# Kernel optimization log

Measured on AMD Instinct MI355X. Metric: run time of the kernel, lower is better.

## Reference

```python
import jax, jax.numpy as jnp
import numpy as np

B, N, C_IN = 32, 1024, 128
F0, F1, F2 = 64, 64, 64
OUT = 10
RATIOS = (0.8, 0.8)
EPS = 1e-5


def setup_inputs() -> dict:
    key = jax.random.key(0)
    ks = jax.random.split(key, 16)
    N_nodes = jax.random.randint(ks[0], (B,), N // 2, N + 1)
    mask = (jnp.arange(N)[None, :] < N_nodes[:, None]).astype(jnp.float32)
    x = jax.random.normal(ks[1], (B, N, C_IN), dtype=jnp.float32)
    # sparse-ish symmetric binary adjacency restricted to valid nodes
    A = (jax.random.uniform(ks[2], (B, N, N)) < 0.02).astype(jnp.float32)
    A = jnp.maximum(A, jnp.swapaxes(A, 1, 2))
    A = A * mask[:, :, None] * mask[:, None, :]
    def lin(k, fi, fo):
        b = 1.0 / np.sqrt(fi)
        kw, kb = jax.random.split(k)
        return (jax.random.uniform(kw, (fi, fo), minval=-b, maxval=b),
                jax.random.uniform(kb, (fo,), minval=-b, maxval=b))
    W0, b0 = lin(ks[3], C_IN, F0)
    W1, b1 = lin(ks[4], F0, F1)
    W2, b2 = lin(ks[5], F1, F2)
    bp0 = 1.0 / np.sqrt(F0)
    p0 = jax.random.uniform(ks[6], (F0, 1), minval=-bp0, maxval=bp0)
    bp1 = 1.0 / np.sqrt(F1)
    p1 = jax.random.uniform(ks[7], (F1, 1), minval=-bp1, maxval=bp1)
    Wfc, bfc = lin(ks[8], F2, OUT)
    return {"x": x, "A": A, "mask": mask, "N_nodes": N_nodes,
            "W0": W0, "b0": b0, "W1": W1, "b1": b1, "W2": W2, "b2": b2,
            "p0": p0, "p1": p1, "Wfc": Wfc, "bfc": bfc}


def _gconv(x, A, W, b):
    # Kipf-Welling normalized Laplacian conv, batched dense
    n = A.shape[1]
    A_hat = A + jnp.eye(n, dtype=A.dtype)[None]
    D = (jnp.sum(A_hat, axis=1) + EPS) ** -0.5  # [B,N]
    L = D[:, :, None] * A_hat * D[:, None, :]
    h = jnp.einsum('bnm,bmc->bnc', L, x) @ W + b
    return jax.nn.relu(h)


def _pool(x, A, mask, N_nodes, p, ratio):
    Bc, Nc, C = x.shape
    y = (x.reshape(Bc * Nc, C) @ p).reshape(Bc, Nc)
    y = y / jnp.sqrt(jnp.sum(p ** 2))
    N_remove = (N_nodes.astype(jnp.float32) * (1.0 - ratio)).astype(N_nodes.dtype)
    # remove the N_remove lowest-scoring valid nodes per graph
    y_eff = jnp.where(mask > 0, y, jnp.inf)
    ranks = jnp.argsort(jnp.argsort(y_eff, axis=1), axis=1)  # ascending rank
    new_mask = mask * (ranks >= N_remove[:, None]).astype(mask.dtype)
    x = x * jnp.tanh(y)[:, :, None] * new_mask[:, :, None]
    A = new_mask[:, :, None] * A * new_mask[:, None, :]
    return x, A, new_mask, N_nodes - N_remove


def reference(x, A, mask, N_nodes, W0, b0, W1, b1, W2, b2, p0, p1, Wfc, bfc):
    x = _gconv(x, A, W0, b0)
    x, A, mask, N_nodes = _pool(x, A, mask, N_nodes, p0, RATIOS[0])
    x = _gconv(x, A, W1, b1)
    x, A, mask, N_nodes = _pool(x, A, mask, N_nodes, p1, RATIOS[1])
    x = _gconv(x, A, W2, b2)
    x = jnp.max(x, axis=1)  # global max pool over nodes [B,F2]
    return x @ Wfc + bfc
```

## Files before the change

### kernel.cpp

```cpp
#include <hip/hip_runtime.h>
#include <cstdint>
#include <cstddef>

#define BB 32
#define NN 1024
#define CIN 128
#define FF 64
#define NOUT 10
#define CAP 128
#define EPSV 1e-5f

__global__ __launch_bounds__(256) void k_front(const float* __restrict__ A,
                                               const float* __restrict__ x,
                                               const float* __restrict__ W0,
                                               unsigned short* __restrict__ adj,
                                               int* __restrict__ cnt,
                                               float* __restrict__ c1,
                                               float* __restrict__ c2,
                                               float* __restrict__ T) {
    __shared__ __align__(16) float Wl[64 * 64];
    int tid = threadIdx.x;
    int wave = tid >> 6, lane = tid & 63;
    if (blockIdx.x >= 8192) {
        int gid = blockIdx.x - 8192;
        int b = gid & 31;
        int cch = gid >> 5;
        int row0 = (b << 10) + cch * 16;
        int rsub = lane >> 4, f0 = (lane & 15) * 4;
        int r = row0 + wave * 4 + rsub;
        const float4* xr = (const float4*)(x + (size_t)r * CIN);
        float4 acc = {0.f, 0.f, 0.f, 0.f};
#pragma unroll
        for (int kc = 0; kc < 2; ++kc) {
            if (kc) __syncthreads();
            for (int t = tid; t < 64 * 16; t += 256)
                ((float4*)Wl)[t] = ((const float4*)W0)[kc * 1024 + t];
            __syncthreads();
#pragma unroll 4
            for (int k4 = 0; k4 < 16; ++k4) {
                float4 xv = xr[kc * 16 + k4];
                float4 w0 = *(const float4*)&Wl[(k4 * 4 + 0) * 64 + f0];
                float4 w1 = *(const float4*)&Wl[(k4 * 4 + 1) * 64 + f0];
                float4 w2 = *(const float4*)&Wl[(k4 * 4 + 2) * 64 + f0];
                float4 w3 = *(const float4*)&Wl[(k4 * 4 + 3) * 64 + f0];
                acc.x += xv.x * w0.x; acc.y += xv.x * w0.y; acc.z += xv.x * w0.z; acc.w += xv.x * w0.w;
                acc.x += xv.y * w1.x; acc.y += xv.y * w1.y; acc.z += xv.y * w1.z; acc.w += xv.y * w1.w;
                acc.x += xv.z * w2.x; acc.y += xv.z * w2.y; acc.z += xv.z * w2.z; acc.w += xv.z * w2.w;
                acc.x += xv.w * w3.x; acc.y += xv.w * w3.y; acc.z += xv.w * w3.z; acc.w += xv.w * w3.w;
            }
        }
        *(float4*)&T[(size_t)r * 64 + f0] = acc;
    } else {
        unsigned short* adjs = ((unsigned short*)Wl) + wave * CAP;
        int r = blockIdx.x * 4 + wave;
        const float4* Arow = (const float4*)(A + (size_t)r * NN);
        float4 v0 = Arow[lane];
        float4 v1 = Arow[64 + lane];
        float4 v2 = Arow[128 + lane];
        float4 v3 = Arow[192 + lane];
        int c = 0;
        unsigned long long lt = (lane == 0) ? 0ULL : ((1ULL << lane) - 1ULL);
        float4 vv[4] = {v0, v1, v2, v3};
#pragma unroll
        for (int it = 0; it < 4; ++it) {
            float4 v = vv[it];
            int j0 = it * 256 + lane * 4;
            unsigned long long m0 = __ballot(v.x != 0.f);
            unsigned long long m1 = __ballot(v.y != 0.f);
            unsigned long long m2 = __ballot(v.z != 0.f);
            unsigned long long m3 = __ballot(v.w != 0.f);
            int before = __popcll(m0 & lt) + __popcll(m1 & lt) +
                         __popcll(m2 & lt) + __popcll(m3 & lt);
            int p = c + before;
            if (v.x != 0.f) { if (p < CAP) adjs[p] = (unsigned short)(j0 + 0); ++p; }
            if (v.y != 0.f) { if (p < CAP) adjs[p] = (unsigned short)(j0 + 1); ++p; }
            if (v.z != 0.f) { if (p < CAP) adjs[p] = (unsigned short)(j0 + 2); ++p; }
            if (v.w != 0.f) { if (p < CAP) adjs[p] = (unsigned short)(j0 + 3); ++p; }
            c += __popcll(m0) + __popcll(m1) + __popcll(m2) + __popcll(m3);
        }
        int cc = (c > CAP) ? CAP : c;
        uint32_t* dst = (uint32_t*)(adj + (size_t)r * CAP);
        if (lane * 2 < cc) dst[lane] = ((const uint32_t*)adjs)[lane];
        if (lane == 0) {
            cnt[r] = cc;
            float D = 1.0f / sqrtf((float)c + 1.0f + EPSV);
            c1[r] = D;
            c2[r] = D * D;
        }
    }
}

__global__ __launch_bounds__(256) void k_mid(const unsigned short* __restrict__ adj,
                                             const int* __restrict__ cnt,
                                             const float* __restrict__ nm,
                                             float* __restrict__ c1, float* __restrict__ c2,
                                             const float* __restrict__ Xin,
                                             const float* __restrict__ W,
                                             const float* __restrict__ y,
                                             float* __restrict__ T) {
    __shared__ __align__(16) float Wl[64 * 64];
    int tid = threadIdx.x;
    if (blockIdx.x >= 8192) {
        int gid = blockIdx.x - 8192;
        int b = gid & 31;
        int cch = gid >> 5;
        int row0 = (b << 10) + cch * 16;
        for (int t = tid; t < 64 * 16; t += 256)
            ((float4*)Wl)[t] = ((const float4*)W)[t];
        __syncthreads();
        int wave = tid >> 6, lane = tid & 63;
        int rsub = lane >> 4, f0 = (lane & 15) * 4;
        int r = row0 + wave * 4 + rsub;
        float sc = tanhf(y[r]) * nm[r];
        const float4* xr = (const float4*)(Xin + (size_t)r * 64);
        float4 acc = {0.f, 0.f, 0.f, 0.f};
#pragma unroll 4
        for (int k4 = 0; k4 < 16; ++k4) {
            float4 xv = xr[k4];
            float4 w0 = *(const float4*)&Wl[(k4 * 4 + 0) * 64 + f0];
            float4 w1 = *(const float4*)&Wl[(k4 * 4 + 1) * 64 + f0];
            float4 w2 = *(const float4*)&Wl[(k4 * 4 + 2) * 64 + f0];
            float4 w3 = *(const float4*)&Wl[(k4 * 4 + 3) * 64 + f0];
            acc.x += xv.x * w0.x; acc.y += xv.x * w0.y; acc.z += xv.x * w0.z; acc.w += xv.x * w0.w;
            acc.x += xv.y * w1.x; acc.y += xv.y * w1.y; acc.z += xv.y * w1.z; acc.w += xv.y * w1.w;
            acc.x += xv.z * w2.x; acc.y += xv.z * w2.y; acc.z += xv.z * w2.z; acc.w += xv.z * w2.w;
            acc.x += xv.w * w3.x; acc.y += xv.w * w3.y; acc.z += xv.w * w3.z; acc.w += xv.w * w3.w;
        }
        acc.x *= sc; acc.y *= sc; acc.z *= sc; acc.w *= sc;
        *(float4*)&T[(size_t)r * 64 + f0] = acc;
    } else {
        int wave = tid >> 6, lane = tid & 63;
        int r = blockIdx.x * 4 + wave;
        int b = r >> 10;
        const unsigned short* arow = adj + (size_t)r * CAP;
        const float* nmb = nm + (b << 10);
        int n = cnt[r];
        float s = 0.f;
        if (lane < n)      s  = nmb[arow[lane]];
        if (lane + 64 < n) s += nmb[arow[lane + 64]];
        for (int sh = 32; sh; sh >>= 1) s += __shfl_xor(s, sh, 64);
        if (lane == 0) {
            float m = nm[r];
            float D = 1.0f / sqrtf(m * s + 1.0f + EPSV);
            c1[r] = m * D;
            c2[r] = D * D;
        }
    }
}

__global__ __launch_bounds__(256) void k_spmm(const unsigned short* __restrict__ adj,
                                              const int* __restrict__ cnt,
                                              const float* __restrict__ c1,
                                              const float* __restrict__ c2,
                                              const float* __restrict__ T,
                                              const float* __restrict__ bias,
                                              float* __restrict__ X,
                                              const float* __restrict__ p,
                                              float* __restrict__ y,
                                              float* __restrict__ gmax) {
    __shared__ __align__(16) float c1s[NN];
    __shared__ float red[4][64];
    int b   = blockIdx.x & 31;
    int cch = blockIdx.x >> 5;
    int tid = threadIdx.x;
    ((float4*)c1s)[tid] = ((const float4*)(c1 + (b << 10)))[tid];
    __syncthreads();
    int wave = tid >> 6, lane = tid & 63;
    int r0 = (b << 10) + cch * 16 + wave * 4;
    const float* Tb = T + ((size_t)(b << 10) << 6);
    float bv = bias[lane];
    float pv = 0.f, ppinv = 0.f;
    if (p != nullptr) {
        pv = p[lane];
        float pp = pv * pv;
        for (int s = 32; s; s >>= 1) pp += __shfl_xor(pp, s, 64);
        ppinv = 1.0f / sqrtf(pp);
    }
    float vmax = 0.f;
#pragma unroll
    for (int rr = 0; rr < 4; ++rr) {
        int r = r0 + rr;
        const unsigned short* arow = adj + (size_t)r * CAP;
        int n = cnt[r];
        float acc0 = 0.f, acc1 = 0.f, acc2 = 0.f, acc3 = 0.f;
        int t = 0;
        for (; t + 4 <= n; t += 4) {
            ushort4 j4 = *(const ushort4*)(arow + t);
            acc0 += c1s[j4.x] * Tb[((int)j4.x << 6) + lane];
            acc1 += c1s[j4.y] * Tb[((int)j4.y << 6) + lane];
            acc2 += c1s[j4.z] * Tb[((int)j4.z << 6) + lane];
            acc3 += c1s[j4.w] * Tb[((int)j4.w << 6) + lane];
        }
        for (; t < n; ++t) {
            int j = arow[t];
            acc0 += c1s[j] * Tb[(j << 6) + lane];
        }
        float acc = (acc0 + acc1) + (acc2 + acc3);
        int rl = r & 1023;
        float o = c1s[rl] * acc + c2[r] * T[((size_t)r << 6) + lane] + bv;
        o = fmaxf(o, 0.f);
        if (X != nullptr) X[((size_t)r << 6) + lane] = o;
        if (p != nullptr) {
            float a = o * pv;
            for (int s = 32; s; s >>= 1) a += __shfl_xor(a, s, 64);
            if (lane == 0) y[r] = a * ppinv;
        }
        vmax = fmaxf(vmax, o);
    }
    if (gmax != nullptr) {
        red[wave][lane] = vmax;
        __syncthreads();
        if (wave == 0) {
            float m = fmaxf(fmaxf(red[0][lane], red[1][lane]),
                            fmaxf(red[2][lane], red[3][lane]));
            atomicMax((int*)&gmax[(b << 6) + lane], __float_as_int(m));
        }
    }
}

__global__ __launch_bounds__(256) void k_rank(const float* __restrict__ y,
                                              const float* __restrict__ maskSrc,
                                              const int* __restrict__ nsrc,
                                              float* __restrict__ nmOut,
                                              int* __restrict__ ncur) {
    __shared__ __align__(16) float yv[NN];
    int b = blockIdx.x >> 4;
    int sub = blockIdx.x & 15;
    int tid = threadIdx.x;
    const float INF = __builtin_inff();
    {
        float4 v = ((const float4*)(y + (b << 10)))[tid];
        float4 m = ((const float4*)(maskSrc + (b << 10)))[tid];
        v.x = (m.x > 0.f) ? v.x : INF;
        v.y = (m.y > 0.f) ? v.y : INF;
        v.z = (m.z > 0.f) ? v.z : INF;
        v.w = (m.w > 0.f) ? v.w : INF;
        ((float4*)yv)[tid] = v;
    }
    int n = nsrc[b];
    const float RM = (float)(1.0 - 0.8);
    int nrem = (int)((float)n * RM);
    if (sub == 0 && tid == 0) ncur[b] = n - nrem;
    __syncthreads();
    int i = (sub << 6) + (tid >> 2);
    int q = tid & 3;
    float yi = yv[i];
    int rank = 0;
    if (yi < INF) {
        const float4* jbase = (const float4*)yv + (q << 6);
        int j0 = q << 8;
#pragma unroll 8
        for (int t = 0; t < 64; ++t) {
            float4 a = jbase[t];
            int j = j0 + t * 4;
            rank += (a.x < yi || (a.x == yi && j     < i)) ? 1 : 0;
            rank += (a.y < yi || (a.y == yi && j + 1 < i)) ? 1 : 0;
            rank += (a.z < yi || (a.z == yi && j + 2 < i)) ? 1 : 0;
            rank += (a.w < yi || (a.w == yi && j + 3 < i)) ? 1 : 0;
        }
    }
    rank += __shfl_xor(rank, 1, 64);
    rank += __shfl_xor(rank, 2, 64);
    if (q == 0) {
        float nmv = (yi < INF && rank >= nrem) ? 1.f : 0.f;
        nmOut[(b << 10) + i] = nmv;
    }
}

__global__ __launch_bounds__(64) void k_fc(const float* __restrict__ gmax,
                                           const float* __restrict__ Wfc,
                                           const float* __restrict__ bfc,
                                           float* __restrict__ out) {
    __shared__ float gl[64];
    int b = blockIdx.x, lane = threadIdx.x;
    gl[lane] = gmax[(b << 6) + lane];
    __syncthreads();
    if (lane < NOUT) {
        float acc = bfc[lane];
        for (int k = 0; k < 64; ++k) acc += gl[k] * Wfc[k * NOUT + lane];
        out[b * NOUT + lane] = acc;
    }
}

extern "C" void kernel_launch(void* const* d_in, const int* in_sizes, int n_in,
                              void* d_out, int out_size, void* d_ws, size_t ws_size,
                              hipStream_t stream) {
    const float* x    = (const float*)d_in[0];
    const float* A    = (const float*)d_in[1];
    const float* mask = (const float*)d_in[2];
    const int*   Nn   = (const int*)d_in[3];
    const float* W0   = (const float*)d_in[4];
    const float* b0   = (const float*)d_in[5];
    const float* W1   = (const float*)d_in[6];
    const float* b1   = (const float*)d_in[7];
    const float* W2   = (const float*)d_in[8];
    const float* b2   = (const float*)d_in[9];
    const float* p0   = (const float*)d_in[10];
    const float* p1   = (const float*)d_in[11];
    const float* Wfc  = (const float*)d_in[12];
    const float* bfc  = (const float*)d_in[13];
    float* out = (float*)d_out;

    char* ws = (char*)d_ws;
    size_t off = 0;
    auto alloc = [&](size_t bytes) -> void* {
        void* p = ws + off;
        off = (off + bytes + 255) & ~(size_t)255;
        return p;
    };
    unsigned short* adj = (unsigned short*)alloc((size_t)BB * NN * CAP * 2);
    int*   cnt  = (int*)  alloc((size_t)BB * NN * 4);
    float* X    = (float*)alloc((size_t)BB * NN * 64 * 4);
    float* T    = (float*)alloc((size_t)BB * NN * 64 * 4);
    float* c1   = (float*)alloc((size_t)BB * NN * 4);
    float* c2   = (float*)alloc((size_t)BB * NN * 4);
    float* y    = (float*)alloc((size_t)BB * NN * 4);
    float* nm0  = (float*)alloc((size_t)BB * NN * 4);
    float* nm1  = (float*)alloc((size_t)BB * NN * 4);
    int*   nc0  = (int*)  alloc((size_t)BB * 4);
    int*   nc1  = (int*)  alloc((size_t)BB * 4);
    float* gmax = (float*)alloc((size_t)BB * 64 * 4);

    hipMemsetAsync(gmax, 0, (size_t)BB * 64 * 4, stream);
    k_front<<<8192 + 2048, 256, 0, stream>>>(A, x, W0, adj, cnt, c1, c2, T);
    k_spmm<<<2048, 256, 0, stream>>>(adj, cnt, c1, c2, T, b0, X, p0, y, nullptr);
    k_rank<<<BB * 16, 256, 0, stream>>>(y, mask, Nn, nm0, nc0);
    k_mid<<<8192 + 2048, 256, 0, stream>>>(adj, cnt, nm0, c1, c2, X, W1, y, T);
    k_spmm<<<2048, 256, 0, stream>>>(adj, cnt, c1, c2, T, b1, X, p1, y, nullptr);
    k_rank<<<BB * 16, 256, 0, stream>>>(y, nm0, nc0, nm1, nc1);
    k_mid<<<8192 + 2048, 256, 0, stream>>>(adj, cnt, nm1, c1, c2, X, W2, y, T);
    k_spmm<<<2048, 256, 0, stream>>>(adj, cnt, c1, c2, T, b2, nullptr, nullptr, nullptr, gmax);
    k_fc<<<BB, 64, 0, stream>>>(gmax, Wfc, bfc, out);
}
```

Measured before the change: 373.1 us.

## Read only upper triangle of symmetric adjacency and scatter mirrored edges atomically

The adjacency extraction now relies on A being symmetric. Each wave handles a pair of rows (i and 1023-i) so the work stays balanced, reads only columns j >= i, and writes the mirrored edge into row j's list through atomic counters. This roughly halves the dominant dense A read. The first-layer degree normalisation is now computed inside the first spmm from the counts, which removes the c1/c2 writes. The cost is many global atomics, and neighbour order within each row is no longer deterministic, so float summation order can change.

```diff
diff --git a/kernel.cpp b/kernel.cpp
--- a/kernel.cpp
+++ b/kernel.cpp
@@ -15,14 +15,12 @@
                                                const float* __restrict__ W0,
                                                unsigned short* __restrict__ adj,
                                                int* __restrict__ cnt,
-                                               float* __restrict__ c1,
-                                               float* __restrict__ c2,
                                                float* __restrict__ T) {
     __shared__ __align__(16) float Wl[64 * 64];
     int tid = threadIdx.x;
     int wave = tid >> 6, lane = tid & 63;
-    if (blockIdx.x >= 8192) {
-        int gid = blockIdx.x - 8192;
+    if (blockIdx.x >= 4096) {
+        int gid = blockIdx.x - 4096;
         int b = gid & 31;
         int cch = gid >> 5;
         int row0 = (b << 10) + cch * 16;
@@ -52,40 +50,52 @@
         *(float4*)&T[(size_t)r * 64 + f0] = acc;
     } else {
         unsigned short* adjs = ((unsigned short*)Wl) + wave * CAP;
-        int r = blockIdx.x * 4 + wave;
-        const float4* Arow = (const float4*)(A + (size_t)r * NN);
-        float4 v0 = Arow[lane];
-        float4 v1 = Arow[64 + lane];
-        float4 v2 = Arow[128 + lane];
-        float4 v3 = Arow[192 + lane];
-        int c = 0;
+        int pairIdx = blockIdx.x * 4 + wave;
+        int b = pairIdx >> 9;
+        int i0 = pairIdx & 511;
+        int rbase = b << 10;
         unsigned long long lt = (lane == 0) ? 0ULL : ((1ULL << lane) - 1ULL);
-        float4 vv[4] = {v0, v1, v2, v3};
 #pragma unroll
-        for (int it = 0; it < 4; ++it) {
-            float4 v = vv[it];
-            int j0 = it * 256 + lane * 4;
-            unsigned long long m0 = __ballot(v.x != 0.f);
-            unsigned long long m1 = __ballot(v.y != 0.f);
-            unsigned long long m2 = __ballot(v.z != 0.f);
-            unsigned long long m3 = __ballot(v.w != 0.f);
-            int before = __popcll(m0 & lt) + __popcll(m1 & lt) +
-                         __popcll(m2 & lt) + __popcll(m3 & lt);
-            int p = c + before;
-            if (v.x != 0.f) { if (p < CAP) adjs[p] = (unsigned short)(j0 + 0); ++p; }
-            if (v.y != 0.f) { if (p < CAP) adjs[p] = (unsigned short)(j0 + 1); ++p; }
-            if (v.z != 0.f) { if (p < CAP) adjs[p] = (unsigned short)(j0 + 2); ++p; }
-            if (v.w != 0.f) { if (p < CAP) adjs[p] = (unsigned short)(j0 + 3); ++p; }
-            c += __popcll(m0) + __popcll(m1) + __popcll(m2) + __popcll(m3);
-        }
-        int cc = (c > CAP) ? CAP : c;
-        uint32_t* dst = (uint32_t*)(adj + (size_t)r * CAP);
-        if (lane * 2 < cc) dst[lane] = ((const uint32_t*)adjs)[lane];
-        if (lane == 0) {
-            cnt[r] = cc;
-            float D = 1.0f / sqrtf((float)c + 1.0f + EPSV);
-            c1[r] = D;
-            c2[r] = D * D;
+        for (int half = 0; half < 2; ++half) {
+            int ii = half ? (1023 - i0) : i0;
+            int r = rbase + ii;
+            const float4* Arow4 = (const float4*)(A + (size_t)r * NN);
+            int startF4 = ii >> 2;
+            int nIt = (256 - startF4 + 63) >> 6;
+            int own = 0;
+            for (int it = 0; it < nIt; ++it) {
+                int f4 = startF4 + it * 64 + lane;
+                float4 v = {0.f, 0.f, 0.f, 0.f};
+                if (f4 < 256) v = Arow4[f4];
+                int j0 = f4 * 4;
+                bool px = (v.x != 0.f) && (j0     >= ii);
+                bool py = (v.y != 0.f) && (j0 + 1 >= ii);
+                bool pz = (v.z != 0.f) && (j0 + 2 >= ii);
+                bool pw = (v.w != 0.f) && (j0 + 3 >= ii);
+                unsigned long long m0 = __ballot(px);
+                unsigned long long m1 = __ballot(py);
+                unsigned long long m2 = __ballot(pz);
+                unsigned long long m3 = __ballot(pw);
+                int before = __popcll(m0 & lt) + __popcll(m1 & lt) +
+                             __popcll(m2 & lt) + __popcll(m3 & lt);
+                int p = own + before;
+                if (px) { if (p < CAP) adjs[p] = (unsigned short)(j0 + 0); ++p; }
+                if (py) { if (p < CAP) adjs[p] = (unsigned short)(j0 + 1); ++p; }
+                if (pz) { if (p < CAP) adjs[p] = (unsigned short)(j0 + 2); ++p; }
+                if (pw) { if (p < CAP) adjs[p] = (unsigned short)(j0 + 3); ++p; }
+                own += __popcll(m0) + __popcll(m1) + __popcll(m2) + __popcll(m3);
+                if (px && j0     > ii) { int q = atomicAdd(&cnt[rbase + j0    ], 1); if (q < CAP) adj[(size_t)(rbase + j0    ) * CAP + q] = (unsigned short)ii; }
+                if (py && j0 + 1 > ii) { int q = atomicAdd(&cnt[rbase + j0 + 1], 1); if (q < CAP) adj[(size_t)(rbase + j0 + 1) * CAP + q] = (unsigned short)ii; }
+                if (pz && j0 + 2 > ii) { int q = atomicAdd(&cnt[rbase + j0 + 2], 1); if (q < CAP) adj[(size_t)(rbase + j0 + 2) * CAP + q] = (unsigned short)ii; }
+                if (pw && j0 + 3 > ii) { int q = atomicAdd(&cnt[rbase + j0 + 3], 1); if (q < CAP) adj[(size_t)(rbase + j0 + 3) * CAP + q] = (unsigned short)ii; }
+            }
+            int base = 0;
+            if (lane == 0 && own > 0) base = atomicAdd(&cnt[r], own);
+            base = __shfl(base, 0, 64);
+            for (int k = lane; k < own; k += 64) {
+                int p = base + k;
+                if (p < CAP) adj[(size_t)r * CAP + p] = adjs[k];
+            }
         }
     }
 }
@@ -134,7 +144,7 @@
         int b = r >> 10;
         const unsigned short* arow = adj + (size_t)r * CAP;
         const float* nmb = nm + (b << 10);
-        int n = cnt[r];
+        int n = cnt[r]; if (n > CAP) n = CAP;
         float s = 0.f;
         if (lane < n)      s  = nmb[arow[lane]];
         if (lane + 64 < n) s += nmb[arow[lane + 64]];
@@ -152,6 +162,7 @@
                                               const int* __restrict__ cnt,
                                               const float* __restrict__ c1,
                                               const float* __restrict__ c2,
+                                              const int* __restrict__ cntc1,
                                               const float* __restrict__ T,
                                               const float* __restrict__ bias,
                                               float* __restrict__ X,
@@ -163,7 +174,17 @@
     int b   = blockIdx.x & 31;
     int cch = blockIdx.x >> 5;
     int tid = threadIdx.x;
-    ((float4*)c1s)[tid] = ((const float4*)(c1 + (b << 10)))[tid];
+    if (cntc1 != nullptr) {
+        int4 cv = ((const int4*)(cntc1 + (b << 10)))[tid];
+        float4 o;
+        o.x = 1.0f / sqrtf((float)cv.x + 1.0f + EPSV);
+        o.y = 1.0f / sqrtf((float)cv.y + 1.0f + EPSV);
+        o.z = 1.0f / sqrtf((float)cv.z + 1.0f + EPSV);
+        o.w = 1.0f / sqrtf((float)cv.w + 1.0f + EPSV);
+        ((float4*)c1s)[tid] = o;
+    } else {
+        ((float4*)c1s)[tid] = ((const float4*)(c1 + (b << 10)))[tid];
+    }
     __syncthreads();
     int wave = tid >> 6, lane = tid & 63;
     int r0 = (b << 10) + cch * 16 + wave * 4;
@@ -181,7 +202,7 @@
     for (int rr = 0; rr < 4; ++rr) {
         int r = r0 + rr;
         const unsigned short* arow = adj + (size_t)r * CAP;
-        int n = cnt[r];
+        int n = cnt[r]; if (n > CAP) n = CAP;
         float acc0 = 0.f, acc1 = 0.f, acc2 = 0.f, acc3 = 0.f;
         int t = 0;
         for (; t + 4 <= n; t += 4) {
@@ -197,7 +218,9 @@
         }
         float acc = (acc0 + acc1) + (acc2 + acc3);
         int rl = r & 1023;
-        float o = c1s[rl] * acc + c2[r] * T[((size_t)r << 6) + lane] + bv;
+        float c1v = c1s[rl];
+        float c2v = (cntc1 != nullptr) ? c1v * c1v : c2[r];
+        float o = c1v * acc + c2v * T[((size_t)r << 6) + lane] + bv;
         o = fmaxf(o, 0.f);
         if (X != nullptr) X[((size_t)r << 6) + lane] = o;
         if (p != nullptr) {
@@ -310,6 +333,7 @@
     };
     unsigned short* adj = (unsigned short*)alloc((size_t)BB * NN * CAP * 2);
     int*   cnt  = (int*)  alloc((size_t)BB * NN * 4);
+    float* gmax = (float*)alloc((size_t)BB * 64 * 4);
     float* X    = (float*)alloc((size_t)BB * NN * 64 * 4);
     float* T    = (float*)alloc((size_t)BB * NN * 64 * 4);
     float* c1   = (float*)alloc((size_t)BB * NN * 4);
@@ -319,16 +343,15 @@
     float* nm1  = (float*)alloc((size_t)BB * NN * 4);
     int*   nc0  = (int*)  alloc((size_t)BB * 4);
     int*   nc1  = (int*)  alloc((size_t)BB * 4);
-    float* gmax = (float*)alloc((size_t)BB * 64 * 4);
-
-    hipMemsetAsync(gmax, 0, (size_t)BB * 64 * 4, stream);
-    k_front<<<8192 + 2048, 256, 0, stream>>>(A, x, W0, adj, cnt, c1, c2, T);
-    k_spmm<<<2048, 256, 0, stream>>>(adj, cnt, c1, c2, T, b0, X, p0, y, nullptr);
+
+    hipMemsetAsync(cnt, 0, (size_t)BB * NN * 4 + (size_t)BB * 64 * 4, stream);
+    k_front<<<4096 + 2048, 256, 0, stream>>>(A, x, W0, adj, cnt, T);
+    k_spmm<<<2048, 256, 0, stream>>>(adj, cnt, nullptr, nullptr, cnt, T, b0, X, p0, y, nullptr);
     k_rank<<<BB * 16, 256, 0, stream>>>(y, mask, Nn, nm0, nc0);
     k_mid<<<8192 + 2048, 256, 0, stream>>>(adj, cnt, nm0, c1, c2, X, W1, y, T);
-    k_spmm<<<2048, 256, 0, stream>>>(adj, cnt, c1, c2, T, b1, X, p1, y, nullptr);
+    k_spmm<<<2048, 256, 0, stream>>>(adj, cnt, c1, c2, nullptr, T, b1, X, p1, y, nullptr);
     k_rank<<<BB * 16, 256, 0, stream>>>(y, nm0, nc0, nm1, nc1);
     k_mid<<<8192 + 2048, 256, 0, stream>>>(adj, cnt, nm1, c1, c2, X, W2, y, T);
-    k_spmm<<<2048, 256, 0, stream>>>(adj, cnt, c1, c2, T, b2, nullptr, nullptr, nullptr, gmax);
+    k_spmm<<<2048, 256, 0, stream>>>(adj, cnt, c1, c2, nullptr, T, b2, nullptr, nullptr, nullptr, gmax);
     k_fc<<<BB, 64, 0, stream>>>(gmax, Wfc, bfc, out);
 }
```

Measured after the change: 387.2 us. +3.8%, slower.
